# Kernel tuning notes

Measured on AMD Instinct MI355X. Metric: run time of the kernel, lower is better.

The kernel has to match this reference:

```python
import jax, jax.numpy as jnp
import numpy as np

B, N, D, H = 8, 1024, 768, 12
HD = D // H
SCALE = HD ** -0.5

def setup_inputs() -> dict:
    key = jax.random.key(0)
    k1, k2, k3, k4 = jax.random.split(key, 4)
    x = jax.random.normal(k1, (B, N, D), dtype=jnp.float32)
    weight = jax.random.uniform(k2, (B, N), dtype=jnp.float32)
    W_qkv = jax.random.normal(k3, (D, 3 * D), dtype=jnp.float32) * (D ** -0.5)
    W_msa = jax.random.normal(k4, (D, D), dtype=jnp.float32) * (D ** -0.5)
    b_msa = jnp.zeros((D,), dtype=jnp.float32)
    return {"x": x, "weight": weight, "W_qkv": W_qkv, "W_msa": W_msa, "b_msa": b_msa}

def reference(x, weight, W_qkv, W_msa, b_msa):
    # QKV projection (no bias), then elementwise per-token gate
    qkv = jnp.einsum('bnd,de->bne', x, W_qkv)          # [B,N,3D]
    qkv = weight[:, :, None] * qkv
    qkv = qkv.reshape(B, N, 3, H, HD).transpose(2, 0, 3, 1, 4)  # [3,B,H,N,hd]
    q, k, v = qkv[0], qkv[1], qkv[2]
    A = jnp.einsum('bhnd,bhmd->bhnm', q, k) * SCALE    # [B,H,N,N]
    A = jax.nn.softmax(A, axis=-1)
    out = jnp.einsum('bhnm,bhmd->bhnd', A, v)          # [B,H,N,hd]
    out = out.transpose(0, 2, 1, 3).reshape(B, N, D)
    return jnp.einsum('bnd,de->bne', out, W_msa) + b_msa
```

## Files before the change

kernel.cpp:

```cpp
#include <hip/hip_runtime.h>
#include <hip/hip_bf16.h>


typedef __attribute__((ext_vector_type(8))) short bf8;
typedef __attribute__((ext_vector_type(4))) float f4;

#define QSCALE 0.1803368801111204f

static __device__ __forceinline__ short bf16_of(float f) {
    union { float f; unsigned u; } a; a.f = f;
    unsigned r = a.u + 0x7FFFu + ((a.u >> 16) & 1u);
    return (short)(r >> 16);
}

static __device__ __forceinline__ unsigned bfpk(float lo, float hi) {
    float2 t; t.x = lo; t.y = hi;
    __hip_bfloat162 b = __float22bfloat162_rn(t);
    union { __hip_bfloat162 b; unsigned u; } c; c.b = b;
    return c.u;
}

static __device__ __forceinline__ void async16(const short* g, short* l) {
    __builtin_amdgcn_global_load_lds(
        (const __attribute__((address_space(1))) void*)g,
        (__attribute__((address_space(3))) void*)l, 16, 0, 0);
}

static __device__ __forceinline__ void transpose64(
        const float* __restrict__ w, short* __restrict__ wt,
        int K, int E, int k0, int e0, int tid, short (*t)[65]) {
#pragma unroll
    for (int p = 0; p < 16; ++p) {
        int idx = p * 256 + tid;
        int r = idx >> 6, c = idx & 63;
        t[r][c] = bf16_of(w[(k0 + r) * E + e0 + c]);
    }
    __syncthreads();
#pragma unroll
    for (int p = 0; p < 16; ++p) {
        int idx = p * 256 + tid;
        int r = idx >> 6, c = idx & 63;
        wt[(e0 + r) * K + k0 + c] = t[c][r];
    }
}

__global__ __launch_bounds__(256) void k_prep(
        const float* __restrict__ x, const float* __restrict__ gate,
        short* __restrict__ xb,
        const float* __restrict__ Wqkv, short* __restrict__ wtq,
        const float* __restrict__ Wmsa, short* __restrict__ wtm) {
    __shared__ short t[64][65];
    const int bid = blockIdx.x, tid = threadIdx.x;
    if (bid < 3072) {
        int i = bid * 256 + tid;
        const float g = gate[i / 96];
        const f4* sp = (const f4*)x;
        f4 a = sp[2 * i], b = sp[2 * i + 1];
        union { bf8 v; short h[8]; } o;
        o.h[0] = bf16_of(a[0] * g); o.h[1] = bf16_of(a[1] * g);
        o.h[2] = bf16_of(a[2] * g); o.h[3] = bf16_of(a[3] * g);
        o.h[4] = bf16_of(b[0] * g); o.h[5] = bf16_of(b[1] * g);
        o.h[6] = bf16_of(b[2] * g); o.h[7] = bf16_of(b[3] * g);
        ((bf8*)xb)[i] = o.v;
    } else if (bid < 3504) {
        int tt = bid - 3072;
        transpose64(Wqkv, wtq, 768, 2304, (tt / 36) * 64, (tt % 36) * 64, tid, t);
    } else {
        int tt = bid - 3504;
        transpose64(Wmsa, wtm, 768, 768, (tt / 12) * 64, (tt % 12) * 64, tid, t);
    }
}

static __device__ __forceinline__ void gemm128(const short* __restrict__ gA,
                                               const short* __restrict__ gB,
                                               short* smem,
                                               f4 acc[4][4]) {
    const int tid = threadIdx.x, lane = tid & 63;
    const int l16 = lane & 15, quad = lane >> 4, rx = l16 & 7;
    const int wm = (tid >> 6) & 1, wn = tid >> 7;

    auto stage = [&](short* S, int k0) {
#pragma unroll
        for (int c = 0; c < 4; ++c) {
            int p = c * 256 + tid;
            int row = p >> 3, slot = p & 7;
            int gc = slot ^ (row & 7);
            async16(gA + row * 768 + k0 + gc * 8, S + p * 8);
            async16(gB + row * 768 + k0 + gc * 8, S + 8192 + p * 8);
        }
    };

    stage(smem, 0);
    for (int it = 0; it < 12; ++it) {
        __builtin_amdgcn_s_waitcnt(0);
        __syncthreads();
        short* Sc = smem + (it & 1) * 16384;
        if (it + 1 < 12) stage(smem + ((it + 1) & 1) * 16384, (it + 1) * 64);
        const short* As = Sc;
        const short* Bs = Sc + 8192;
#pragma unroll
        for (int ks = 0; ks < 2; ++ks) {
            bf8 af[4], bfr[4];
#pragma unroll
            for (int mt = 0; mt < 4; ++mt)
                af[mt] = *(const bf8*)(As + (wm * 64 + mt * 16 + l16) * 64 +
                                       (((ks * 4 + quad) ^ rx) * 8));
#pragma unroll
            for (int nt = 0; nt < 4; ++nt)
                bfr[nt] = *(const bf8*)(Bs + (wn * 64 + nt * 16 + l16) * 64 +
                                        (((ks * 4 + quad) ^ rx) * 8));
#pragma unroll
            for (int mt = 0; mt < 4; ++mt)
#pragma unroll
                for (int nt = 0; nt < 4; ++nt)
                    acc[mt][nt] = __builtin_amdgcn_mfma_f32_16x16x32_bf16(
                        af[mt], bfr[nt], acc[mt][nt], 0, 0, 0);
        }
    }
    __syncthreads();
}

__global__ __launch_bounds__(512, 2) void k_gemm_qkv(
        const short* __restrict__ xb, const short* __restrict__ wtq,
        short* __restrict__ qb, short* __restrict__ kb, short* __restrict__ vt) {
    __shared__ short lds[69632];
    const int tid = threadIdx.x, lane = tid & 63;
    const int l16 = lane & 15, quad = lane >> 4, rx = l16 & 7;
    const int wv = tid >> 6, wm = wv >> 1, wn = wv & 1;

    const int wg = blockIdx.x;
    const int swz = (wg & 7) * 32 + (wg >> 3);
    const int mI = swz >> 3, nI = swz & 7;
    const int m0 = mI * 256, n0 = nI * 288;

    const short* gA = xb + m0 * 768;
    const short* gB = wtq + n0 * 768;

    auto stageA = [&](int buf, int half, int k0) {
        short* dst = lds + buf * 34816 + half * 8192;
        const short* src = gA + half * 98304 + k0;
#pragma unroll
        for (int j = 0; j < 2; ++j) {
            int p = j * 512 + tid;
            int row = p >> 3;
            int gc = (p & 7) ^ (row & 7);
            async16(src + row * 768 + gc * 8, dst + p * 8);
        }
    };
    auto stageB = [&](int buf, int half, int k0) {
        short* dst = lds + buf * 34816 + 16384 + half * 9216;
        const short* src = gB + half * 110592 + k0;
#pragma unroll
        for (int j = 0; j < 2; ++j) {
            int p = j * 512 + tid;
            int row = p >> 3;
            int gc = (p & 7) ^ (row & 7);
            async16(src + row * 768 + gc * 8, dst + p * 8);
        }
        if (tid < 128) {
            int p = 1024 + tid;
            int row = p >> 3;
            int gc = (p & 7) ^ (row & 7);
            async16(src + row * 768 + gc * 8, dst + p * 8);
        }
    };

    f4 z = {0.f, 0.f, 0.f, 0.f};
    f4 acc[4][9];
#pragma unroll
    for (int mf = 0; mf < 4; ++mf)
#pragma unroll
        for (int nf = 0; nf < 9; ++nf) acc[mf][nf] = z;

    stageA(0, 0, 0); stageA(0, 1, 0);
    stageB(0, 0, 0); stageB(0, 1, 0);
    stageB(1, 0, 64);
    if (wv < 2) asm volatile("s_waitcnt vmcnt(3)" ::: "memory");
    else        asm volatile("s_waitcnt vmcnt(2)" ::: "memory");
    __builtin_amdgcn_s_barrier();

#pragma unroll 2
    for (int t = 0; t < 12; ++t) {
        const short* Ab = lds + (t & 1) * 34816;
        const short* Bb = Ab + 16384;
        auto rdA = [&](int mf, int ks) {
            return *(const bf8*)(Ab + (wm * 64 + mf * 16 + l16) * 64 +
                                 (((ks * 4 + quad) ^ rx) << 3));
        };
        auto rdB = [&](int nf, int ks) {
            return *(const bf8*)(Bb + (wn * 144 + nf * 16 + l16) * 64 +
                                 (((ks * 4 + quad) ^ rx) << 3));
        };
        bf8 af[4][2], bfr[9][2];

#pragma unroll
        for (int mf = 0; mf < 2; ++mf) { af[mf][0] = rdA(mf, 0); af[mf][1] = rdA(mf, 1); }
#pragma unroll
        for (int nf = 0; nf < 5; ++nf) { bfr[nf][0] = rdB(nf, 0); bfr[nf][1] = rdB(nf, 1); }
        if (t < 11) stageB((t + 1) & 1, 1, (t + 1) * 64);
        __builtin_amdgcn_s_barrier();
        __builtin_amdgcn_s_setprio(1);
#pragma unroll
        for (int mf = 0; mf < 2; ++mf)
#pragma unroll
            for (int nf = 0; nf < 5; ++nf) {
                acc[mf][nf] = __builtin_amdgcn_mfma_f32_16x16x32_bf16(
                    af[mf][0], bfr[nf][0], acc[mf][nf], 0, 0, 0);
                acc[mf][nf] = __builtin_amdgcn_mfma_f32_16x16x32_bf16(
                    af[mf][1], bfr[nf][1], acc[mf][nf], 0, 0, 0);
            }
        __builtin_amdgcn_s_setprio(0);
        __builtin_amdgcn_s_barrier();

#pragma unroll
        for (int mf = 2; mf < 4; ++mf) { af[mf][0] = rdA(mf, 0); af[mf][1] = rdA(mf, 1); }
        if (t < 11) stageA((t + 1) & 1, 0, (t + 1) * 64);
        __builtin_amdgcn_s_barrier();
        __builtin_amdgcn_s_setprio(1);
#pragma unroll
        for (int mf = 2; mf < 4; ++mf)
#pragma unroll
            for (int nf = 0; nf < 5; ++nf) {
                acc[mf][nf] = __builtin_amdgcn_mfma_f32_16x16x32_bf16(
                    af[mf][0], bfr[nf][0], acc[mf][nf], 0, 0, 0);
                acc[mf][nf] = __builtin_amdgcn_mfma_f32_16x16x32_bf16(
                    af[mf][1], bfr[nf][1], acc[mf][nf], 0, 0, 0);
            }
        __builtin_amdgcn_s_setprio(0);
        __builtin_amdgcn_s_barrier();

#pragma unroll
        for (int nf = 5; nf < 9; ++nf) { bfr[nf][0] = rdB(nf, 0); bfr[nf][1] = rdB(nf, 1); }
        if (t < 11) stageA((t + 1) & 1, 1, (t + 1) * 64);
        __builtin_amdgcn_s_barrier();
        __builtin_amdgcn_s_setprio(1);
#pragma unroll
        for (int mf = 0; mf < 2; ++mf)
#pragma unroll
            for (int nf = 5; nf < 9; ++nf) {
                acc[mf][nf] = __builtin_amdgcn_mfma_f32_16x16x32_bf16(
                    af[mf][0], bfr[nf][0], acc[mf][nf], 0, 0, 0);
                acc[mf][nf] = __builtin_amdgcn_mfma_f32_16x16x32_bf16(
                    af[mf][1], bfr[nf][1], acc[mf][nf], 0, 0, 0);
            }
        __builtin_amdgcn_s_setprio(0);
        __builtin_amdgcn_s_barrier();

        if (t < 10) stageB(t & 1, 0, (t + 2) * 64);
        __builtin_amdgcn_s_barrier();
        __builtin_amdgcn_s_setprio(1);
#pragma unroll
        for (int mf = 2; mf < 4; ++mf)
#pragma unroll
            for (int nf = 5; nf < 9; ++nf) {
                acc[mf][nf] = __builtin_amdgcn_mfma_f32_16x16x32_bf16(
                    af[mf][0], bfr[nf][0], acc[mf][nf], 0, 0, 0);
                acc[mf][nf] = __builtin_amdgcn_mfma_f32_16x16x32_bf16(
                    af[mf][1], bfr[nf][1], acc[mf][nf], 0, 0, 0);
            }
        __builtin_amdgcn_s_setprio(0);
        if (t < 10) {
            if (wv < 2) asm volatile("s_waitcnt vmcnt(3)" ::: "memory");
            else        asm volatile("s_waitcnt vmcnt(2)" ::: "memory");
        } else if (t == 10) {
            asm volatile("s_waitcnt vmcnt(0)" ::: "memory");
        }
        __builtin_amdgcn_s_barrier();
    }

    const int bI = m0 >> 10, nn0 = m0 & 1023;
#pragma unroll
    for (int nf = 0; nf < 9; ++nf) {
        const int ct = n0 + wn * 144 + nf * 16;
        if (ct < 1536) {
            const int which = (ct >= 768) ? 1 : 0;
            const int h = (ct - which * 768) >> 6;
            const int hd = (ct & 63) + l16;
            short* dst = (which ? kb : qb) + ((bI * 12 + h) * 1024) * 64 + hd;
#pragma unroll
            for (int mf = 0; mf < 4; ++mf)
#pragma unroll
                for (int r = 0; r < 4; ++r) {
                    const int nn = nn0 + wm * 64 + mf * 16 + quad * 4 + r;
                    const float val = acc[mf][nf][r];
                    dst[nn * 64] = bf16_of(which ? val : val * QSCALE);
                }
        }
    }
    const int vstart = (n0 >= 1536) ? n0 : 1536;
    const int npass = (n0 + 288 > vstart) ? (n0 + 288 - vstart) / 96 : 0;
    for (int p = 0; p < npass; ++p) {
        __syncthreads();
        const int c0 = vstart + p * 96;
#pragma unroll
        for (int nf = 0; nf < 9; ++nf) {
            const int ct = n0 + wn * 144 + nf * 16;
            if (ct >= c0 && ct < c0 + 96) {
                const int lc = ct - c0 + l16;
#pragma unroll
                for (int mf = 0; mf < 4; ++mf)
#pragma unroll
                    for (int r = 0; r < 4; ++r) {
                        const int rl = wm * 64 + mf * 16 + quad * 4 + r;
                        lds[lc * 264 + rl] = bf16_of(acc[mf][nf][r]);
                    }
            }
        }
        __syncthreads();
        const int vg0 = c0 - 1536;
#pragma unroll
        for (int u = 0; u < 6; ++u) {
            const int idx = u * 512 + tid;
            const int lc = idx >> 5, ck = idx & 31;
            const int vg = vg0 + lc;
            const int h = vg >> 6, hd = vg & 63;
            bf8 vv = *(const bf8*)(lds + lc * 264 + ck * 8);
            *(bf8*)(vt + ((bI * 12 + h) * 64 + hd) * 1024 + nn0 + ck * 8) = vv;
        }
    }
}

__global__ __launch_bounds__(256) void k_gemm_final(
        const short* __restrict__ attn, const short* __restrict__ wtm,
        const float* __restrict__ bias, float* __restrict__ out) {
    __shared__ short smem[32768];
    const int lane = threadIdx.x & 63;
    const int l16 = lane & 15, quad = lane >> 4;
    const int wm = (threadIdx.x >> 6) & 1, wn = threadIdx.x >> 7;
    const int m0 = blockIdx.y * 128, n0 = blockIdx.x * 128;
    f4 z = {0.f, 0.f, 0.f, 0.f};
    f4 acc[4][4] = {{z,z,z,z},{z,z,z,z},{z,z,z,z},{z,z,z,z}};
    gemm128(attn + m0 * 768, wtm + n0 * 768, smem, acc);
#pragma unroll
    for (int mt = 0; mt < 4; ++mt) {
#pragma unroll
        for (int r = 0; r < 4; ++r) {
            const int row = m0 + wm * 64 + mt * 16 + quad * 4 + r;
#pragma unroll
            for (int nt = 0; nt < 4; ++nt) {
                const int e = n0 + wn * 64 + nt * 16 + l16;
                out[row * 768 + e] = acc[mt][nt][r] + bias[e];
            }
        }
    }
}

__global__ __launch_bounds__(256, 3) void k_attn(const short* __restrict__ qb,
                                                 const short* __restrict__ kb,
                                                 const short* __restrict__ vt,
                                                 short* __restrict__ attn) {
    __shared__ short Ks[2][4096];
    __shared__ short Vs[2][4096];
    const int tid = threadIdx.x, wave = tid >> 6, lane = tid & 63;
    const int l16 = lane & 15, quad = lane >> 4;
    const int bh = blockIdx.x;
    const int b = bh / 12, h = bh - b * 12;
    const int m_base = blockIdx.y * 128 + wave * 32;
    const short* qh = qb + bh * 65536;
    const short* kh = kb + bh * 65536;
    const short* vh = vt + bh * 65536;

    const int rA = ((l16 >> 2) << 3) + (l16 & 3);
    const int fK = (((rA >> 3) & 1) << 2) + (rA & 3);
    const int sK = (quad ^ fK) * 8;
    const int oAlo = rA * 64 + sK;
    const int oAhi = rA * 64 + (sK ^ 32);
    const int oBlo = oAlo + 256, oBhi = oAhi + 256;
    const int fV = (((l16 >> 3) & 1) << 2) + (l16 & 3);
    const int oV = l16 * 64 + ((quad ^ fV) * 8);

    const short* qp0 = qh + (m_base + l16) * 64 + quad * 8;
    bf8 qf00 = *(const bf8*)(qp0);
    bf8 qf01 = *(const bf8*)(qp0 + 32);
    const short* qp1 = qp0 + 16 * 64;
    bf8 qf10 = *(const bf8*)(qp1);
    bf8 qf11 = *(const bf8*)(qp1 + 32);

    union { bf8 v; short h[8]; } onef;
#pragma unroll
    for (int i = 0; i < 8; ++i) onef.h[i] = (short)0x3F80;

    f4 z = {0.f, 0.f, 0.f, 0.f};
    f4 acc0[4] = {z, z, z, z};
    f4 acc1[4] = {z, z, z, z};
    f4 accl0 = z, accl1 = z;

    auto stage = [&](int buf, int j0) {
#pragma unroll
        for (int j = 0; j < 2; ++j) {
            int idx = j * 256 + tid;
            int row = idx >> 3;
            int fr = (((row >> 3) & 1) << 2) + (row & 3);
            int gc = (idx & 7) ^ fr;
            async16(kh + (j0 + row) * 64 + gc * 8, Ks[buf] + idx * 8);
            async16(vh + row * 1024 + j0 + gc * 8, Vs[buf] + idx * 8);
        }
    };

    stage(0, 0);
    int cur = 0;
    for (int it = 0; it < 16; ++it) {
        __builtin_amdgcn_s_waitcnt(0);
        __syncthreads();
        if (it + 1 < 16) stage(cur ^ 1, (it + 1) * 64);
        const short* Kc = Ks[cur];
        const short* Vc = Vs[cur];

#pragma unroll
        for (int jj = 0; jj < 64; jj += 32) {
            const short* kjj = Kc + jj * 64;
            bf8 kAlo = *(const bf8*)(kjj + oAlo);
            bf8 kAhi = *(const bf8*)(kjj + oAhi);
            bf8 kBlo = *(const bf8*)(kjj + oBlo);
            bf8 kBhi = *(const bf8*)(kjj + oBhi);
            bf8 vf0 = *(const bf8*)(Vc + 0 * 1024 + (oV ^ (jj ? 32 : 0)));
            bf8 vf1 = *(const bf8*)(Vc + 1 * 1024 + (oV ^ (jj ? 32 : 0)));
            bf8 vf2 = *(const bf8*)(Vc + 2 * 1024 + (oV ^ (jj ? 32 : 0)));
            bf8 vf3 = *(const bf8*)(Vc + 3 * 1024 + (oV ^ (jj ? 32 : 0)));

            {
                f4 sA = z, sB = z;
                sA = __builtin_amdgcn_mfma_f32_16x16x32_bf16(kAlo, qf00, sA, 0, 0, 0);
                sA = __builtin_amdgcn_mfma_f32_16x16x32_bf16(kAhi, qf01, sA, 0, 0, 0);
                sB = __builtin_amdgcn_mfma_f32_16x16x32_bf16(kBlo, qf00, sB, 0, 0, 0);
                sB = __builtin_amdgcn_mfma_f32_16x16x32_bf16(kBhi, qf01, sB, 0, 0, 0);
                float a0 = __builtin_amdgcn_exp2f(sA[0]);
                float a1 = __builtin_amdgcn_exp2f(sA[1]);
                float a2 = __builtin_amdgcn_exp2f(sA[2]);
                float a3 = __builtin_amdgcn_exp2f(sA[3]);
                float b0 = __builtin_amdgcn_exp2f(sB[0]);
                float b1 = __builtin_amdgcn_exp2f(sB[1]);
                float b2 = __builtin_amdgcn_exp2f(sB[2]);
                float b3 = __builtin_amdgcn_exp2f(sB[3]);
                union { bf8 v; unsigned u[4]; } p;
                p.u[0] = bfpk(a0, a1); p.u[1] = bfpk(a2, a3);
                p.u[2] = bfpk(b0, b1); p.u[3] = bfpk(b2, b3);
                accl0 = __builtin_amdgcn_mfma_f32_16x16x32_bf16(
                    onef.v, p.v, accl0, 0, 0, 0);
                acc0[0] = __builtin_amdgcn_mfma_f32_16x16x32_bf16(vf0, p.v, acc0[0], 0, 0, 0);
                acc0[1] = __builtin_amdgcn_mfma_f32_16x16x32_bf16(vf1, p.v, acc0[1], 0, 0, 0);
                acc0[2] = __builtin_amdgcn_mfma_f32_16x16x32_bf16(vf2, p.v, acc0[2], 0, 0, 0);
                acc0[3] = __builtin_amdgcn_mfma_f32_16x16x32_bf16(vf3, p.v, acc0[3], 0, 0, 0);
            }
            {
                f4 sA = z, sB = z;
                sA = __builtin_amdgcn_mfma_f32_16x16x32_bf16(kAlo, qf10, sA, 0, 0, 0);
                sA = __builtin_amdgcn_mfma_f32_16x16x32_bf16(kAhi, qf11, sA, 0, 0, 0);
                sB = __builtin_amdgcn_mfma_f32_16x16x32_bf16(kBlo, qf10, sB, 0, 0, 0);
                sB = __builtin_amdgcn_mfma_f32_16x16x32_bf16(kBhi, qf11, sB, 0, 0, 0);
                float a0 = __builtin_amdgcn_exp2f(sA[0]);
                float a1 = __builtin_amdgcn_exp2f(sA[1]);
                float a2 = __builtin_amdgcn_exp2f(sA[2]);
                float a3 = __builtin_amdgcn_exp2f(sA[3]);
                float b0 = __builtin_amdgcn_exp2f(sB[0]);
                float b1 = __builtin_amdgcn_exp2f(sB[1]);
                float b2 = __builtin_amdgcn_exp2f(sB[2]);
                float b3 = __builtin_amdgcn_exp2f(sB[3]);
                union { bf8 v; unsigned u[4]; } p;
                p.u[0] = bfpk(a0, a1); p.u[1] = bfpk(a2, a3);
                p.u[2] = bfpk(b0, b1); p.u[3] = bfpk(b2, b3);
                accl1 = __builtin_amdgcn_mfma_f32_16x16x32_bf16(
                    onef.v, p.v, accl1, 0, 0, 0);
                acc1[0] = __builtin_amdgcn_mfma_f32_16x16x32_bf16(vf0, p.v, acc1[0], 0, 0, 0);
                acc1[1] = __builtin_amdgcn_mfma_f32_16x16x32_bf16(vf1, p.v, acc1[1], 0, 0, 0);
                acc1[2] = __builtin_amdgcn_mfma_f32_16x16x32_bf16(vf2, p.v, acc1[2], 0, 0, 0);
                acc1[3] = __builtin_amdgcn_mfma_f32_16x16x32_bf16(vf3, p.v, acc1[3], 0, 0, 0);
            }
        }
        cur ^= 1;
    }

    const float inv0 = 1.f / accl0[0];
    const float inv1 = 1.f / accl1[0];
    const int row0 = (b << 10) + m_base + l16;
    short* op0 = attn + row0 * 768 + h * 64 + quad * 4;
    short* op1 = op0 + 16 * 768;
#pragma unroll
    for (int dt = 0; dt < 4; ++dt)
#pragma unroll
        for (int r = 0; r < 4; ++r) {
            op0[dt * 16 + r] = bf16_of(acc0[dt][r] * inv0);
            op1[dt * 16 + r] = bf16_of(acc1[dt][r] * inv1);
        }
}

extern "C" void kernel_launch(void* const* d_in, const int* in_sizes, int n_in,
                              void* d_out, int out_size, void* d_ws, size_t ws_size,
                              hipStream_t stream) {
    const float* x    = (const float*)d_in[0];
    const float* gate = (const float*)d_in[1];
    const float* Wqkv = (const float*)d_in[2];
    const float* Wmsa = (const float*)d_in[3];
    const float* bmsa = (const float*)d_in[4];
    float* out = (float*)d_out;

    char* ws = (char*)d_ws;
    short* xb  = (short*)(ws);
    short* wtq = (short*)(ws + 12582912);
    short* wtm = (short*)(ws + 16121856);
    short* qb  = (short*)(ws + 17301504);
    short* kb  = (short*)(ws + 29884416);
    short* vt  = (short*)(ws + 42467328);
    short* attn = xb;

    k_prep<<<3648, 256, 0, stream>>>(x, gate, xb, Wqkv, wtq, Wmsa, wtm);
    k_gemm_qkv<<<256, 512, 0, stream>>>(xb, wtq, qb, kb, vt);
    k_attn<<<dim3(96, 8), 256, 0, stream>>>(qb, kb, vt, attn);
    k_gemm_final<<<dim3(6, 64), 256, 0, stream>>>(attn, wtm, bmsa, out);
}
```

Baseline: 175.7 us.

## Split QKV GEMM into two passes over column fragments to cut accumulators

The QKV GEMM kernel now runs the full K loop twice, once for fragments 0-4 and once for 5-8 of each wave's 144-column slice. Each pass holds fewer accumulators, which lowers register pressure. The pipeline is simplified to stage both halves of A and B each iteration with a full vmcnt(0) wait, and the V transpose epilogue is done per fragment. The cost is reloading the A tile twice from global memory, a weaker load/compute overlap, and more barriers in the epilogue.

```diff
diff --git a/kernel.cpp b/kernel.cpp
--- a/kernel.cpp
+++ b/kernel.cpp
@@ -120,21 +120,14 @@
     __syncthreads();
 }
 
-__global__ __launch_bounds__(512, 2) void k_gemm_qkv(
-        const short* __restrict__ xb, const short* __restrict__ wtq,
-        short* __restrict__ qb, short* __restrict__ kb, short* __restrict__ vt) {
-    __shared__ short lds[69632];
+template<int NFLO, int NFN>
+static __device__ __forceinline__ void qkv_pass(
+        const short* __restrict__ gA, const short* __restrict__ gB,
+        short* lds, short* __restrict__ qb, short* __restrict__ kb,
+        short* __restrict__ vt, int m0, int n0) {
     const int tid = threadIdx.x, lane = tid & 63;
     const int l16 = lane & 15, quad = lane >> 4, rx = l16 & 7;
     const int wv = tid >> 6, wm = wv >> 1, wn = wv & 1;
-
-    const int wg = blockIdx.x;
-    const int swz = (wg & 7) * 32 + (wg >> 3);
-    const int mI = swz >> 3, nI = swz & 7;
-    const int m0 = mI * 256, n0 = nI * 288;
-
-    const short* gA = xb + m0 * 768;
-    const short* gB = wtq + n0 * 768;
 
     auto stageA = [&](int buf, int half, int k0) {
         short* dst = lds + buf * 34816 + half * 8192;
@@ -166,17 +159,16 @@
     };
 
     f4 z = {0.f, 0.f, 0.f, 0.f};
-    f4 acc[4][9];
+    f4 acc[4][NFN];
 #pragma unroll
     for (int mf = 0; mf < 4; ++mf)
 #pragma unroll
-        for (int nf = 0; nf < 9; ++nf) acc[mf][nf] = z;
-
+        for (int nf = 0; nf < NFN; ++nf) acc[mf][nf] = z;
+
+    __syncthreads();
     stageA(0, 0, 0); stageA(0, 1, 0);
     stageB(0, 0, 0); stageB(0, 1, 0);
-    stageB(1, 0, 64);
-    if (wv < 2) asm volatile("s_waitcnt vmcnt(3)" ::: "memory");
-    else        asm volatile("s_waitcnt vmcnt(2)" ::: "memory");
+    asm volatile("s_waitcnt vmcnt(0)" ::: "memory");
     __builtin_amdgcn_s_barrier();
 
 #pragma unroll 2
@@ -188,22 +180,23 @@
                                  (((ks * 4 + quad) ^ rx) << 3));
         };
         auto rdB = [&](int nf, int ks) {
-            return *(const bf8*)(Bb + (wn * 144 + nf * 16 + l16) * 64 +
+            return *(const bf8*)(Bb + (wn * 144 + (NFLO + nf) * 16 + l16) * 64 +
                                  (((ks * 4 + quad) ^ rx) << 3));
         };
-        bf8 af[4][2], bfr[9][2];
+        bf8 af[4][2], bfr[NFN][2];
 
 #pragma unroll
         for (int mf = 0; mf < 2; ++mf) { af[mf][0] = rdA(mf, 0); af[mf][1] = rdA(mf, 1); }
 #pragma unroll
-        for (int nf = 0; nf < 5; ++nf) { bfr[nf][0] = rdB(nf, 0); bfr[nf][1] = rdB(nf, 1); }
-        if (t < 11) stageB((t + 1) & 1, 1, (t + 1) * 64);
+        for (int nf = 0; nf < NFN; ++nf) { bfr[nf][0] = rdB(nf, 0); bfr[nf][1] = rdB(nf, 1); }
+        if (t < 11) { stageA((t + 1) & 1, 0, (t + 1) * 64);
+                      stageB((t + 1) & 1, 0, (t + 1) * 64); }
         __builtin_amdgcn_s_barrier();
         __builtin_amdgcn_s_setprio(1);
 #pragma unroll
         for (int mf = 0; mf < 2; ++mf)
 #pragma unroll
-            for (int nf = 0; nf < 5; ++nf) {
+            for (int nf = 0; nf < NFN; ++nf) {
                 acc[mf][nf] = __builtin_amdgcn_mfma_f32_16x16x32_bf16(
                     af[mf][0], bfr[nf][0], acc[mf][nf], 0, 0, 0);
                 acc[mf][nf] = __builtin_amdgcn_mfma_f32_16x16x32_bf16(
@@ -214,69 +207,34 @@
 
 #pragma unroll
         for (int mf = 2; mf < 4; ++mf) { af[mf][0] = rdA(mf, 0); af[mf][1] = rdA(mf, 1); }
-        if (t < 11) stageA((t + 1) & 1, 0, (t + 1) * 64);
+        if (t < 11) { stageA((t + 1) & 1, 1, (t + 1) * 64);
+                      stageB((t + 1) & 1, 1, (t + 1) * 64); }
         __builtin_amdgcn_s_barrier();
         __builtin_amdgcn_s_setprio(1);
 #pragma unroll
         for (int mf = 2; mf < 4; ++mf)
 #pragma unroll
-            for (int nf = 0; nf < 5; ++nf) {
+            for (int nf = 0; nf < NFN; ++nf) {
                 acc[mf][nf] = __builtin_amdgcn_mfma_f32_16x16x32_bf16(
                     af[mf][0], bfr[nf][0], acc[mf][nf], 0, 0, 0);
                 acc[mf][nf] = __builtin_amdgcn_mfma_f32_16x16x32_bf16(
                     af[mf][1], bfr[nf][1], acc[mf][nf], 0, 0, 0);
             }
         __builtin_amdgcn_s_setprio(0);
+        if (t < 11) asm volatile("s_waitcnt vmcnt(0)" ::: "memory");
         __builtin_amdgcn_s_barrier();
-
-#pragma unroll
-        for (int nf = 5; nf < 9; ++nf) { bfr[nf][0] = rdB(nf, 0); bfr[nf][1] = rdB(nf, 1); }
-        if (t < 11) stageA((t + 1) & 1, 1, (t + 1) * 64);
-        __builtin_amdgcn_s_barrier();
-        __builtin_amdgcn_s_setprio(1);
-#pragma unroll
-        for (int mf = 0; mf < 2; ++mf)
-#pragma unroll
-            for (int nf = 5; nf < 9; ++nf) {
-                acc[mf][nf] = __builtin_amdgcn_mfma_f32_16x16x32_bf16(
-                    af[mf][0], bfr[nf][0], acc[mf][nf], 0, 0, 0);
-                acc[mf][nf] = __builtin_amdgcn_mfma_f32_16x16x32_bf16(
-                    af[mf][1], bfr[nf][1], acc[mf][nf], 0, 0, 0);
-            }
-        __builtin_amdgcn_s_setprio(0);
-        __builtin_amdgcn_s_barrier();
-
-        if (t < 10) stageB(t & 1, 0, (t + 2) * 64);
-        __builtin_amdgcn_s_barrier();
-        __builtin_amdgcn_s_setprio(1);
-#pragma unroll
-        for (int mf = 2; mf < 4; ++mf)
-#pragma unroll
-            for (int nf = 5; nf < 9; ++nf) {
-                acc[mf][nf] = __builtin_amdgcn_mfma_f32_16x16x32_bf16(
-                    af[mf][0], bfr[nf][0], acc[mf][nf], 0, 0, 0);
-                acc[mf][nf] = __builtin_amdgcn_mfma_f32_16x16x32_bf16(
-                    af[mf][1], bfr[nf][1], acc[mf][nf], 0, 0, 0);
-            }
-        __builtin_amdgcn_s_setprio(0);
-        if (t < 10) {
-            if (wv < 2) asm volatile("s_waitcnt vmcnt(3)" ::: "memory");
-            else        asm volatile("s_waitcnt vmcnt(2)" ::: "memory");
-        } else if (t == 10) {
-            asm volatile("s_waitcnt vmcnt(0)" ::: "memory");
-        }
-        __builtin_amdgcn_s_barrier();
     }
 
     const int bI = m0 >> 10, nn0 = m0 & 1023;
 #pragma unroll
-    for (int nf = 0; nf < 9; ++nf) {
-        const int ct = n0 + wn * 144 + nf * 16;
+    for (int nf = 0; nf < NFN; ++nf) {
+        const int ctg = NFLO + nf;
+        const int ct = n0 + wn * 144 + ctg * 16;
         if (ct < 1536) {
             const int which = (ct >= 768) ? 1 : 0;
             const int h = (ct - which * 768) >> 6;
             const int hd = (ct & 63) + l16;
-            short* dst = (which ? kb : qb) + ((bI * 12 + h) * 1024) * 64 + hd;
+            short* dst = (which ? kb : qb) + (bI * 12 + h) * 65536 + hd;
 #pragma unroll
             for (int mf = 0; mf < 4; ++mf)
 #pragma unroll
@@ -286,38 +244,51 @@
                     dst[nn * 64] = bf16_of(which ? val : val * QSCALE);
                 }
         }
-    }
-    const int vstart = (n0 >= 1536) ? n0 : 1536;
-    const int npass = (n0 + 288 > vstart) ? (n0 + 288 - vstart) / 96 : 0;
-    for (int p = 0; p < npass; ++p) {
-        __syncthreads();
-        const int c0 = vstart + p * 96;
-#pragma unroll
-        for (int nf = 0; nf < 9; ++nf) {
-            const int ct = n0 + wn * 144 + nf * 16;
-            if (ct >= c0 && ct < c0 + 96) {
-                const int lc = ct - c0 + l16;
+        const bool v0 = (n0 + ctg * 16) >= 1536;
+        const bool v1 = (n0 + 144 + ctg * 16) >= 1536;
+        if (v1) {
+            __syncthreads();
+            if (ct >= 1536) {
 #pragma unroll
                 for (int mf = 0; mf < 4; ++mf)
 #pragma unroll
                     for (int r = 0; r < 4; ++r) {
                         const int rl = wm * 64 + mf * 16 + quad * 4 + r;
-                        lds[lc * 264 + rl] = bf16_of(acc[mf][nf][r]);
+                        lds[(wn * 16 + l16) * 264 + rl] = bf16_of(acc[mf][nf][r]);
                     }
             }
-        }
-        __syncthreads();
-        const int vg0 = c0 - 1536;
-#pragma unroll
-        for (int u = 0; u < 6; ++u) {
-            const int idx = u * 512 + tid;
-            const int lc = idx >> 5, ck = idx & 31;
-            const int vg = vg0 + lc;
-            const int h = vg >> 6, hd = vg & 63;
-            bf8 vv = *(const bf8*)(lds + lc * 264 + ck * 8);
-            *(bf8*)(vt + ((bI * 12 + h) * 64 + hd) * 1024 + nn0 + ck * 8) = vv;
-        }
-    }
+            __syncthreads();
+            const int nch = v0 ? 2 : 1;
+#pragma unroll
+            for (int u = 0; u < 2; ++u) {
+                if (u < nch) {
+                    const int idx = u * 512 + tid;
+                    const int colIdx = idx >> 5, ck = idx & 31;
+                    const int hsel = v0 ? (colIdx >> 4) : 1;
+                    const int lcol = colIdx & 15;
+                    const int ctv = n0 + hsel * 144 + ctg * 16 + lcol;
+                    const int vg = ctv - 1536;
+                    const int h = vg >> 6, hd = vg & 63;
+                    bf8 vv = *(const bf8*)(lds + (hsel * 16 + lcol) * 264 + ck * 8);
+                    *(bf8*)(vt + ((bI * 12 + h) * 64 + hd) * 1024 + nn0 + ck * 8) = vv;
+                }
+            }
+        }
+    }
+}
+
+__global__ __launch_bounds__(512, 2) void k_gemm_qkv(
+        const short* __restrict__ xb, const short* __restrict__ wtq,
+        short* __restrict__ qb, short* __restrict__ kb, short* __restrict__ vt) {
+    __shared__ short lds[69632];
+    const int wg = blockIdx.x;
+    const int swz = (wg & 7) * 32 + (wg >> 3);
+    const int mI = swz >> 3, nI = swz & 7;
+    const int m0 = mI * 256, n0 = nI * 288;
+    const short* gA = xb + m0 * 768;
+    const short* gB = wtq + n0 * 768;
+    qkv_pass<0, 5>(gA, gB, lds, qb, kb, vt, m0, n0);
+    qkv_pass<5, 4>(gA, gB, lds, qb, kb, vt, m0, n0);
 }
 
 __global__ __launch_bounds__(256) void k_gemm_final(
```

After: 184.6 us. +5.1%, slower.
